# Kernel optimization log

Hardware: AMD Instinct MI355X
Metric: run time of the kernel (lower is better)

## Reference

```python
import jax, jax.numpy as jnp
import numpy as np

N = 20000   # nodes
E = 320000  # directed edges (before self-loops)
D = 64      # input_dim
H = 10      # GAT heads
HD = H * D  # 640
NEG_SLOPE = 0.2


def setup_inputs() -> dict:
    key = jax.random.key(0)
    ks = jax.random.split(key, 10)
    return {
        "x": jax.random.normal(ks[0], (N, D), jnp.float32),
        "W_gat": jax.random.normal(ks[1], (D, HD), jnp.float32) / np.sqrt(D).astype(np.float32),
        "att_src": jax.random.normal(ks[2], (H, D), jnp.float32) / np.sqrt(D).astype(np.float32),
        "att_dst": jax.random.normal(ks[3], (H, D), jnp.float32) / np.sqrt(D).astype(np.float32),
        "b_gat": jnp.zeros((HD,), jnp.float32),
        "W_gcn": jax.random.normal(ks[4], (HD, HD), jnp.float32) / np.sqrt(HD).astype(np.float32),
        "b_gcn": jnp.zeros((HD,), jnp.float32),
        "W1": jax.random.normal(ks[5], (2 * HD, 1500), jnp.float32) / np.sqrt(2 * HD).astype(np.float32),
        "b1": jnp.zeros((1500,), jnp.float32),
        "W2": jax.random.normal(ks[6], (1500, 10), jnp.float32) / np.sqrt(1500).astype(np.float32),
        "b2": jnp.zeros((10,), jnp.float32),
        "edge_index": jax.random.randint(ks[7], (2, E), 0, N, dtype=jnp.int64),
    }


def _forward(x, W_gat, att_src, att_dst, b_gat, W_gcn, b_gcn, W1, b1, W2, b2, edge_index):
    n = x.shape[0]
    # add self-loops (PyG default for both GATConv and GCNConv)
    loop = jnp.arange(n, dtype=edge_index.dtype)
    ei = jnp.concatenate([edge_index, jnp.stack([loop, loop])], axis=1)
    src, dst = ei[0], ei[1]

    # ---- GATConv(D -> D, heads=H, concat) ----
    xl = (x @ W_gat).reshape(n, H, D)                      # [N,H,D]
    a_src = jnp.einsum('nhd,hd->nh', xl, att_src)          # [N,H]
    a_dst = jnp.einsum('nhd,hd->nh', xl, att_dst)          # [N,H]
    alpha = jax.nn.leaky_relu(a_src[src] + a_dst[dst], NEG_SLOPE)  # [E',H]
    m = jax.ops.segment_max(alpha, dst, num_segments=n)    # segment softmax over incoming edges
    ex = jnp.exp(alpha - m[dst])
    den = jax.ops.segment_sum(ex, dst, num_segments=n)
    w = ex / (den[dst] + 1e-16)                            # [E',H]
    msg = xl[src] * w[:, :, None]                          # [E',H,D]
    x1 = jax.ops.segment_sum(msg, dst, num_segments=n).reshape(n, HD) + b_gat
    x1 = jax.nn.relu(x1)

    # ---- GCNConv(HD -> HD), symmetric norm with self-loops ----
    deg = jax.ops.segment_sum(jnp.ones(ei.shape[1], x.dtype), dst, num_segments=n)
    dinv = jnp.where(deg > 0, jax.lax.rsqrt(deg), 0.0)
    norm = dinv[src] * dinv[dst]                           # [E']
    xw = x1 @ W_gcn                                        # [N,HD]
    x2 = jax.ops.segment_sum(xw[src] * norm[:, None], dst, num_segments=n) + b_gcn
    x2 = jax.nn.relu(x2)

    # ---- global max/mean pool (batch=None -> single graph) + MLP head ----
    pooled = jnp.concatenate([x2.max(axis=0, keepdims=True),
                              x2.mean(axis=0, keepdims=True)], axis=1)  # [1, 2*HD]
    h = jax.nn.relu(pooled @ W1 + b1)
    # dropout is identity in eval mode
    return h @ W2 + b2                                     # [1, 10]


def reference(x, W_gat, att_src, att_dst, b_gat, W_gcn, b_gcn, W1, b1, W2, b2, edge_index):
    return _forward(x, W_gat, att_src, att_dst, b_gat, W_gcn, b_gcn, W1, b1, W2, b2, edge_index)
```

## Files before the change

kernel.cpp:

```cpp
#include <hip/hip_runtime.h>
#include <hip/hip_bf16.h>
#include <math.h>

#define NN 20000
#define DD 64
#define HH 10
#define HDIM 640
#define NEG 0.2f
#define H1 1500
#define ASTRIDE 12
#define BKK 128

typedef _Float16 half8 __attribute__((ext_vector_type(8)));
typedef _Float16 half4v __attribute__((ext_vector_type(4)));
typedef _Float16 half2v __attribute__((ext_vector_type(2)));
typedef float f32x4 __attribute__((ext_vector_type(4)));

__global__ __launch_bounds__(256) void k_cvtT(const float* __restrict__ W,
                                              _Float16* __restrict__ WT,
                                              int rows, int cols)
{
    __shared__ float t[32][33];
    const int bx = blockIdx.x, by = blockIdx.y;
    const int lx = threadIdx.x & 31, ly = threadIdx.x >> 5;
    #pragma unroll
    for (int i = ly; i < 32; i += 8)
        t[i][lx] = W[(size_t)(by * 32 + i) * cols + bx * 32 + lx];
    __syncthreads();
    #pragma unroll
    for (int j = ly; j < 32; j += 8)
        WT[(size_t)(bx * 32 + j) * rows + by * 32 + lx] = (_Float16)t[lx][j];
}

__global__ __launch_bounds__(256) void k_gemm1(
    const float* __restrict__ x, const _Float16* __restrict__ WgT,
    const float* __restrict__ att_s, const float* __restrict__ att_d,
    _Float16* __restrict__ xl, float* __restrict__ a_src, float* __restrict__ a_dst)
{
    __shared__ _Float16 As[128][72];
    __shared__ _Float16 Bs[64][72];
    const int tid = threadIdx.x;
    const int m0 = blockIdx.x * 128;
    const int h  = blockIdx.y;
    const int n0 = h * 64;

    {
        const int row = tid >> 1, ch = (tid & 1) * 32;
        const int gr = m0 + row;
        if (gr < NN) {
            const float* xp = &x[(size_t)gr * DD + ch];
            #pragma unroll
            for (int i = 0; i < 8; ++i) {
                const float4 v = *(const float4*)&xp[i * 4];
                half4v o = {(_Float16)v.x, (_Float16)v.y, (_Float16)v.z, (_Float16)v.w};
                *(half4v*)&As[row][ch + i * 4] = o;
            }
        } else {
            const half8 z = {0, 0, 0, 0, 0, 0, 0, 0};
            #pragma unroll
            for (int i = 0; i < 4; ++i) *(half8*)&As[row][ch + i * 8] = z;
        }
    }
    {
        const int row = tid >> 2, part = (tid & 3) * 16;
        const _Float16* wp = &WgT[(size_t)(n0 + row) * DD + part];
        *(half8*)&Bs[row][part]     = *(const half8*)&wp[0];
        *(half8*)&Bs[row][part + 8] = *(const half8*)&wp[8];
    }
    __syncthreads();

    const int lane = tid & 63, wave = tid >> 6;
    const int l15 = lane & 15, quad = lane >> 4;
    f32x4 acc[2][4];
    #pragma unroll
    for (int r = 0; r < 2; ++r)
        #pragma unroll
        for (int c = 0; c < 4; ++c) acc[r][c] = (f32x4){0.f, 0.f, 0.f, 0.f};

    #pragma unroll
    for (int ks = 0; ks < 2; ++ks) {
        const half8 a0 = *(const half8*)&As[wave * 32 + l15][ks * 32 + quad * 8];
        const half8 a1 = *(const half8*)&As[wave * 32 + 16 + l15][ks * 32 + quad * 8];
        #pragma unroll
        for (int c = 0; c < 4; ++c) {
            const half8 b = *(const half8*)&Bs[c * 16 + l15][ks * 32 + quad * 8];
            acc[0][c] = __builtin_amdgcn_mfma_f32_16x16x32_f16(a0, b, acc[0][c], 0, 0, 0);
            acc[1][c] = __builtin_amdgcn_mfma_f32_16x16x32_f16(a1, b, acc[1][c], 0, 0, 0);
        }
    }

    float asv[4], adv[4];
    #pragma unroll
    for (int c = 0; c < 4; ++c) {
        asv[c] = att_s[h * DD + c * 16 + l15];
        adv[c] = att_d[h * DD + c * 16 + l15];
    }
    #pragma unroll
    for (int r = 0; r < 2; ++r) {
        float ps[4] = {0.f, 0.f, 0.f, 0.f}, pd[4] = {0.f, 0.f, 0.f, 0.f};
        #pragma unroll
        for (int c = 0; c < 4; ++c)
            #pragma unroll
            for (int g = 0; g < 4; ++g) {
                ps[g] = fmaf(acc[r][c][g], asv[c], ps[g]);
                pd[g] = fmaf(acc[r][c][g], adv[c], pd[g]);
            }
        #pragma unroll
        for (int m = 1; m <= 8; m <<= 1)
            #pragma unroll
            for (int g = 0; g < 4; ++g) {
                ps[g] += __shfl_xor(ps[g], m);
                pd[g] += __shfl_xor(pd[g], m);
            }
        #pragma unroll
        for (int c = 0; c < 4; ++c)
            #pragma unroll
            for (int g = 0; g < 4; ++g) {
                const int row = m0 + wave * 32 + r * 16 + quad * 4 + g;
                if (row < NN)
                    xl[(size_t)row * HDIM + n0 + c * 16 + l15] = (_Float16)acc[r][c][g];
            }
        if (l15 == 0)
            #pragma unroll
            for (int g = 0; g < 4; ++g) {
                const int row = m0 + wave * 32 + r * 16 + quad * 4 + g;
                if (row < NN) {
                    a_src[(size_t)row * ASTRIDE + h] = ps[g];
                    a_dst[(size_t)row * ASTRIDE + h] = pd[g];
                }
            }
    }
}

__global__ void k_count(const int* __restrict__ ei, int E, int* __restrict__ cnt)
{
    const int e = blockIdx.x * blockDim.x + threadIdx.x;
    if (e >= E + NN) return;
    const int d = (e < E) ? ei[E + e] : (e - E);
    atomicAdd(&cnt[d], 1);
}

__global__ __launch_bounds__(1024) void k_scan(const int* __restrict__ cnt,
                                               int* __restrict__ rowptr,
                                               float* __restrict__ dinv)
{
    __shared__ int sh[1024];
    const int t = threadIdx.x;
    const int CH = 20;
    const int base = t * CH;
    int loc[CH];
    int s = 0;
    #pragma unroll
    for (int i = 0; i < CH; ++i) {
        const int idx = base + i;
        const int c = (idx < NN) ? cnt[idx] : 0;
        loc[i] = s; s += c;
    }
    sh[t] = s; __syncthreads();
    for (int off = 1; off < 1024; off <<= 1) {
        const int v = (t >= off) ? sh[t - off] : 0;
        __syncthreads();
        sh[t] += v;
        __syncthreads();
    }
    const int prev = (t == 0) ? 0 : sh[t - 1];
    #pragma unroll
    for (int i = 0; i < CH; ++i) {
        const int idx = base + i;
        if (idx < NN) {
            rowptr[idx] = prev + loc[i];
            dinv[idx]   = rsqrtf((float)cnt[idx]);
        }
    }
    if (t == 1023) rowptr[NN] = sh[1023];
}

__global__ void k_fill(const int* __restrict__ ei, int E,
                       const int* __restrict__ rowptr,
                       int* __restrict__ cursor, int* __restrict__ csr,
                       int* __restrict__ dstv,
                       const float* __restrict__ dinv, float* __restrict__ wn)
{
    const int e = blockIdx.x * blockDim.x + threadIdx.x;
    if (e >= E + NN) return;
    int s, d;
    if (e < E) { s = ei[e]; d = ei[E + e]; } else { s = d = e - E; }
    const int pos = atomicAdd(&cursor[d], 1);
    const int idx = rowptr[d] + pos;
    csr[idx]  = s;
    dstv[idx] = d;
    wn[idx]   = dinv[s] * dinv[d];
}

__global__ void k_stat(const int* __restrict__ csr, const int* __restrict__ dstv,
                       const float* __restrict__ aS, const float* __restrict__ aD,
                       float* __restrict__ wgat, int EP)
{
    const int j = blockIdx.x * blockDim.x + threadIdx.x;
    if (j >= EP) return;
    const int s = csr[j], d = dstv[j];
    const f32x4 s0 = *(const f32x4*)&aS[(size_t)s * ASTRIDE];
    const f32x4 s1 = *(const f32x4*)&aS[(size_t)s * ASTRIDE + 4];
    const float2 s2 = *(const float2*)&aS[(size_t)s * ASTRIDE + 8];
    const f32x4 d0 = *(const f32x4*)&aD[(size_t)d * ASTRIDE];
    const f32x4 d1 = *(const f32x4*)&aD[(size_t)d * ASTRIDE + 4];
    const float2 d2 = *(const float2*)&aD[(size_t)d * ASTRIDE + 8];
    const float av[10] = {s0.x + d0.x, s0.y + d0.y, s0.z + d0.z, s0.w + d0.w,
                          s1.x + d1.x, s1.y + d1.y, s1.z + d1.z, s1.w + d1.w,
                          s2.x + d2.x, s2.y + d2.y};
    float* wp = &wgat[(size_t)j * HH];
    #pragma unroll
    for (int h = 0; h < 10; ++h) {
        float a = av[h];
        a = (a >= 0.f) ? a : NEG * a;
        wp[h] = __expf(a);
    }
}

__global__ __launch_bounds__(256) void k_gat_gather(
    const int* __restrict__ rowptr, const int* __restrict__ csr,
    const float* __restrict__ wgat, const _Float16* __restrict__ xl,
    const float* __restrict__ b_gat, _Float16* __restrict__ x1)
{
    const int wave = threadIdx.x >> 6, lane = threadIdx.x & 63;
    const int n = blockIdx.x * 4 + wave;
    const int c0 = lane * 8;
    const int h0 = lane >> 3;
    const bool dual = (lane < 16);
    const int c1 = 512 + lane * 8;
    const int h1 = 8 + (lane >> 3);

    float acc0[8], acc1[8], ws0 = 0.f, ws1 = 0.f;
    #pragma unroll
    for (int i = 0; i < 8; ++i) { acc0[i] = 0.f; acc1[i] = 0.f; }

    const int j0 = rowptr[n], j1 = rowptr[n + 1];
    int j = j0;
    for (; j + 3 < j1; j += 4) {
        const int sA = csr[j], sB = csr[j + 1], sC = csr[j + 2], sD = csr[j + 3];
        const float wA0 = wgat[(size_t)(j + 0) * HH + h0];
        const float wB0 = wgat[(size_t)(j + 1) * HH + h0];
        const float wC0 = wgat[(size_t)(j + 2) * HH + h0];
        const float wD0 = wgat[(size_t)(j + 3) * HH + h0];
        ws0 += wA0 + wB0 + wC0 + wD0;
        const half8 vA0 = *(const half8*)&xl[(size_t)sA * HDIM + c0];
        const half8 vB0 = *(const half8*)&xl[(size_t)sB * HDIM + c0];
        const half8 vC0 = *(const half8*)&xl[(size_t)sC * HDIM + c0];
        const half8 vD0 = *(const half8*)&xl[(size_t)sD * HDIM + c0];
        #pragma unroll
        for (int i = 0; i < 8; ++i) {
            acc0[i] = fmaf(wA0, (float)vA0[i], acc0[i]);
            acc0[i] = fmaf(wB0, (float)vB0[i], acc0[i]);
            acc0[i] = fmaf(wC0, (float)vC0[i], acc0[i]);
            acc0[i] = fmaf(wD0, (float)vD0[i], acc0[i]);
        }
        if (dual) {
            const float wA1 = wgat[(size_t)(j + 0) * HH + h1];
            const float wB1 = wgat[(size_t)(j + 1) * HH + h1];
            const float wC1 = wgat[(size_t)(j + 2) * HH + h1];
            const float wD1 = wgat[(size_t)(j + 3) * HH + h1];
            ws1 += wA1 + wB1 + wC1 + wD1;
            const half8 vA1 = *(const half8*)&xl[(size_t)sA * HDIM + c1];
            const half8 vB1 = *(const half8*)&xl[(size_t)sB * HDIM + c1];
            const half8 vC1 = *(const half8*)&xl[(size_t)sC * HDIM + c1];
            const half8 vD1 = *(const half8*)&xl[(size_t)sD * HDIM + c1];
            #pragma unroll
            for (int i = 0; i < 8; ++i) {
                acc1[i] = fmaf(wA1, (float)vA1[i], acc1[i]);
                acc1[i] = fmaf(wB1, (float)vB1[i], acc1[i]);
                acc1[i] = fmaf(wC1, (float)vC1[i], acc1[i]);
                acc1[i] = fmaf(wD1, (float)vD1[i], acc1[i]);
            }
        }
    }
    for (; j < j1; ++j) {
        const int sA = csr[j];
        const float wA0 = wgat[(size_t)j * HH + h0];
        ws0 += wA0;
        const half8 vA0 = *(const half8*)&xl[(size_t)sA * HDIM + c0];
        #pragma unroll
        for (int i = 0; i < 8; ++i) acc0[i] = fmaf(wA0, (float)vA0[i], acc0[i]);
        if (dual) {
            const float wA1 = wgat[(size_t)j * HH + h1];
            ws1 += wA1;
            const half8 vA1 = *(const half8*)&xl[(size_t)sA * HDIM + c1];
            #pragma unroll
            for (int i = 0; i < 8; ++i) acc1[i] = fmaf(wA1, (float)vA1[i], acc1[i]);
        }
    }

    {
        const float rr = 1.f / (ws0 + 1e-16f);
        const float4 ba = *(const float4*)&b_gat[c0];
        const float4 bb = *(const float4*)&b_gat[c0 + 4];
        const float bv[8] = {ba.x, ba.y, ba.z, ba.w, bb.x, bb.y, bb.z, bb.w};
        half8 o;
        #pragma unroll
        for (int i = 0; i < 8; ++i) {
            const float v = fmaf(acc0[i], rr, bv[i]);
            o[i] = (_Float16)((v > 0.f) ? v : 0.f);
        }
        *(half8*)&x1[(size_t)n * HDIM + c0] = o;
    }
    if (dual) {
        const float rr = 1.f / (ws1 + 1e-16f);
        const float4 ba = *(const float4*)&b_gat[c1];
        const float4 bb = *(const float4*)&b_gat[c1 + 4];
        const float bv[8] = {ba.x, ba.y, ba.z, ba.w, bb.x, bb.y, bb.z, bb.w};
        half8 o;
        #pragma unroll
        for (int i = 0; i < 8; ++i) {
            const float v = fmaf(acc1[i], rr, bv[i]);
            o[i] = (_Float16)((v > 0.f) ? v : 0.f);
        }
        *(half8*)&x1[(size_t)n * HDIM + c1] = o;
    }
}

__global__ __launch_bounds__(256) void k_gemm2(const _Float16* __restrict__ X,
                                               const _Float16* __restrict__ Wbt,
                                               _Float16* __restrict__ Y)
{
    __shared__ _Float16 Bs[128 * BKK];
    const int tid = threadIdx.x;
    const int lane = tid & 63, wave = tid >> 6;
    const int l15 = lane & 15, quad = lane >> 4;
    const int m0 = blockIdx.x * 128 + wave * 32;
    const int n0 = blockIdx.y * 128;
    const int l7 = l15 & 7;

    f32x4 acc[2][8];
    #pragma unroll
    for (int r = 0; r < 2; ++r)
        #pragma unroll
        for (int c = 0; c < 8; ++c) acc[r][c] = (f32x4){0.f, 0.f, 0.f, 0.f};

    const int jrow = lane >> 4;
    const int jchunk = lane & 15;

    const _Float16* a0p = &X[(size_t)(m0 + l15) * HDIM + quad * 8];
    const _Float16* a1p = a0p + (size_t)16 * HDIM;

    for (int kb = 0; kb < HDIM; kb += BKK) {
        #pragma unroll
        for (int i = 0; i < 8; ++i) {
            const int r = (wave * 8 + i) * 4 + jrow;
            const int ck = jchunk ^ (r & 7);
            const _Float16* src = &Wbt[(size_t)(n0 + r) * HDIM + kb + ck * 8];
            __builtin_amdgcn_global_load_lds(
                (const __attribute__((address_space(1))) void*)src,
                (__attribute__((address_space(3))) void*)&Bs[(size_t)(wave * 8 + i) * 512],
                16, 0, 0);
        }
        half8 a0[4], a1[4];
        #pragma unroll
        for (int ks = 0; ks < 4; ++ks) {
            a0[ks] = *(const half8*)(a0p + kb + ks * 32);
            a1[ks] = *(const half8*)(a1p + kb + ks * 32);
        }
        __syncthreads();
        #pragma unroll
        for (int ks = 0; ks < 4; ++ks) {
            #pragma unroll
            for (int c = 0; c < 8; ++c) {
                const int br = c * 16 + l15;
                const int ck = (4 * ks + quad) ^ l7;
                const half8 b = *(const half8*)&Bs[(size_t)br * BKK + ck * 8];
                acc[0][c] = __builtin_amdgcn_mfma_f32_16x16x32_f16(a0[ks], b, acc[0][c], 0, 0, 0);
                acc[1][c] = __builtin_amdgcn_mfma_f32_16x16x32_f16(a1[ks], b, acc[1][c], 0, 0, 0);
            }
        }
        __syncthreads();
    }

    #pragma unroll
    for (int r = 0; r < 2; ++r) {
        #pragma unroll
        for (int c = 0; c < 8; ++c) {
            #pragma unroll
            for (int g = 0; g < 4; ++g) {
                const int row = m0 + r * 16 + quad * 4 + g;
                if (row < NN)
                    Y[(size_t)row * HDIM + n0 + c * 16 + l15] = (_Float16)acc[r][c][g];
            }
        }
    }
}

__global__ __launch_bounds__(256) void k_gcn_gather(
    const int* __restrict__ rowptr, const int* __restrict__ csr,
    const float* __restrict__ wn, const _Float16* __restrict__ xw,
    const float* __restrict__ b_gcn, _Float16* __restrict__ x2)
{
    const int wave = threadIdx.x >> 6, lane = threadIdx.x & 63;
    const int n = blockIdx.x * 4 + wave;
    const int c0 = lane * 8;
    const bool dual = (lane < 16);
    const int c1 = 512 + lane * 8;

    float acc0[8], acc1[8];
    #pragma unroll
    for (int i = 0; i < 8; ++i) { acc0[i] = 0.f; acc1[i] = 0.f; }

    const int j0 = rowptr[n], j1 = rowptr[n + 1];
    int j = j0;
    for (; j + 3 < j1; j += 4) {
        const int sA = csr[j], sB = csr[j + 1], sC = csr[j + 2], sD = csr[j + 3];
        const float wA = wn[j], wB = wn[j + 1], wC = wn[j + 2], wD = wn[j + 3];
        const half8 vA0 = *(const half8*)&xw[(size_t)sA * HDIM + c0];
        const half8 vB0 = *(const half8*)&xw[(size_t)sB * HDIM + c0];
        const half8 vC0 = *(const half8*)&xw[(size_t)sC * HDIM + c0];
        const half8 vD0 = *(const half8*)&xw[(size_t)sD * HDIM + c0];
        #pragma unroll
        for (int i = 0; i < 8; ++i) {
            acc0[i] = fmaf(wA, (float)vA0[i], acc0[i]);
            acc0[i] = fmaf(wB, (float)vB0[i], acc0[i]);
            acc0[i] = fmaf(wC, (float)vC0[i], acc0[i]);
            acc0[i] = fmaf(wD, (float)vD0[i], acc0[i]);
        }
        if (dual) {
            const half8 vA1 = *(const half8*)&xw[(size_t)sA * HDIM + c1];
            const half8 vB1 = *(const half8*)&xw[(size_t)sB * HDIM + c1];
            const half8 vC1 = *(const half8*)&xw[(size_t)sC * HDIM + c1];
            const half8 vD1 = *(const half8*)&xw[(size_t)sD * HDIM + c1];
            #pragma unroll
            for (int i = 0; i < 8; ++i) {
                acc1[i] = fmaf(wA, (float)vA1[i], acc1[i]);
                acc1[i] = fmaf(wB, (float)vB1[i], acc1[i]);
                acc1[i] = fmaf(wC, (float)vC1[i], acc1[i]);
                acc1[i] = fmaf(wD, (float)vD1[i], acc1[i]);
            }
        }
    }
    for (; j < j1; ++j) {
        const int sA = csr[j];
        const float wA = wn[j];
        const half8 vA0 = *(const half8*)&xw[(size_t)sA * HDIM + c0];
        #pragma unroll
        for (int i = 0; i < 8; ++i) acc0[i] = fmaf(wA, (float)vA0[i], acc0[i]);
        if (dual) {
            const half8 vA1 = *(const half8*)&xw[(size_t)sA * HDIM + c1];
            #pragma unroll
            for (int i = 0; i < 8; ++i) acc1[i] = fmaf(wA, (float)vA1[i], acc1[i]);
        }
    }

    {
        const float4 ba = *(const float4*)&b_gcn[c0];
        const float4 bb = *(const float4*)&b_gcn[c0 + 4];
        const float bv[8] = {ba.x, ba.y, ba.z, ba.w, bb.x, bb.y, bb.z, bb.w};
        half8 o;
        #pragma unroll
        for (int i = 0; i < 8; ++i) {
            const float v = acc0[i] + bv[i];
            o[i] = (_Float16)((v > 0.f) ? v : 0.f);
        }
        *(half8*)&x2[(size_t)n * HDIM + c0] = o;
    }
    if (dual) {
        const float4 ba = *(const float4*)&b_gcn[c1];
        const float4 bb = *(const float4*)&b_gcn[c1 + 4];
        const float bv[8] = {ba.x, ba.y, ba.z, ba.w, bb.x, bb.y, bb.z, bb.w};
        half8 o;
        #pragma unroll
        for (int i = 0; i < 8; ++i) {
            const float v = acc1[i] + bv[i];
            o[i] = (_Float16)((v > 0.f) ? v : 0.f);
        }
        *(half8*)&x2[(size_t)n * HDIM + c1] = o;
    }
}

__global__ __launch_bounds__(64) void k_pool(const _Float16* __restrict__ x2,
                                             float* __restrict__ pmax,
                                             float* __restrict__ psum)
{
    const int t = threadIdx.x;
    const int col = blockIdx.x * 128 + t * 2;
    const int nb = blockIdx.y;
    float mx0 = 0.f, mx1 = 0.f, s0 = 0.f, s1 = 0.f;
    const int nend = nb * 250 + 250;
    for (int n = nb * 250; n < nend; ++n) {
        const half2v v = *(const half2v*)&x2[(size_t)n * HDIM + col];
        const float v0 = (float)v.x, v1 = (float)v.y;
        mx0 = fmaxf(mx0, v0); mx1 = fmaxf(mx1, v1);
        s0 += v0; s1 += v1;
    }
    atomicMax((int*)&pmax[col],     __float_as_int(mx0));
    atomicMax((int*)&pmax[col + 1], __float_as_int(mx1));
    atomicAdd(&psum[col],     s0);
    atomicAdd(&psum[col + 1], s1);
}

__global__ __launch_bounds__(256) void k_mlp1(const float* __restrict__ pmax,
                                              const float* __restrict__ psum,
                                              const float* __restrict__ W1,
                                              float* __restrict__ hacc)
{
    __shared__ float pl[80];
    const int t = threadIdx.x;
    const int i0 = blockIdx.y * 80;
    if (t < 80) {
        const int i = i0 + t;
        pl[t] = (i < HDIM) ? pmax[i] : psum[i - HDIM] * (1.0f / NN);
    }
    __syncthreads();
    const int j = blockIdx.x * 256 + t;
    if (j >= H1) return;
    float acc = 0.f;
    #pragma unroll 8
    for (int i = 0; i < 80; ++i)
        acc = fmaf(pl[i], W1[(size_t)(i0 + i) * H1 + j], acc);
    atomicAdd(&hacc[j], acc);
}

__global__ __launch_bounds__(256) void k_mlp2(const float* __restrict__ hacc,
                                              const float* __restrict__ b1,
                                              const float* __restrict__ W2,
                                              const float* __restrict__ b2,
                                              float* __restrict__ out)
{
    __shared__ float hsh[H1];
    __shared__ float red[256];
    const int t = threadIdx.x;
    for (int i = t; i < H1; i += 256) {
        const float v = hacc[i] + b1[i];
        hsh[i] = (v > 0.f) ? v : 0.f;
    }
    __syncthreads();
    float acc[10];
    #pragma unroll
    for (int k = 0; k < 10; ++k) acc[k] = 0.f;
    for (int i = t; i < H1; i += 256) {
        const float h = hsh[i];
        #pragma unroll
        for (int k = 0; k < 10; ++k) acc[k] = fmaf(h, W2[i * 10 + k], acc[k]);
    }
    for (int k = 0; k < 10; ++k) {
        red[t] = acc[k]; __syncthreads();
        for (int s2 = 128; s2 > 0; s2 >>= 1) {
            if (t < s2) red[t] += red[t + s2];
            __syncthreads();
        }
        if (t == 0) out[k] = red[0] + b2[k];
        __syncthreads();
    }
}

extern "C" void kernel_launch(void* const* d_in, const int* in_sizes, int n_in,
                              void* d_out, int out_size, void* d_ws, size_t ws_size,
                              hipStream_t stream)
{
    const float* x     = (const float*)d_in[0];
    const float* Wg    = (const float*)d_in[1];
    const float* att_s = (const float*)d_in[2];
    const float* att_d = (const float*)d_in[3];
    const float* b_gat = (const float*)d_in[4];
    const float* Wgcn  = (const float*)d_in[5];
    const float* b_gcn = (const float*)d_in[6];
    const float* W1    = (const float*)d_in[7];
    const float* b1    = (const float*)d_in[8];
    const float* W2    = (const float*)d_in[9];
    const float* b2    = (const float*)d_in[10];
    const int*   ei    = (const int*)d_in[11];
    const int E = in_sizes[11] / 2;
    const int EP = E + NN;
    float* out = (float*)d_out;

    char* wsp = (char*)d_ws;
    size_t off = 0;
    auto alc = [&](size_t b) { void* p = wsp + off; off += (b + 255) & ~(size_t)255; return p; };
    _Float16* bufA = (_Float16*)alc((size_t)NN * HDIM * 2);
    _Float16* bufB = (_Float16*)alc((size_t)NN * HDIM * 2);
    float* aS     = (float*)alc((size_t)NN * ASTRIDE * 4);
    float* aD     = (float*)alc((size_t)NN * ASTRIDE * 4);
    int*   rowptr = (int*)alc((size_t)(NN + 1) * 4);
    int*   csr    = (int*)alc((size_t)EP * 4);
    int*   dstv   = (int*)alc((size_t)EP * 4);
    float* dinv   = (float*)alc((size_t)NN * 4);
    float* wn     = (float*)alc((size_t)EP * 4);
    float* wgat   = (float*)alc((size_t)EP * HH * 4);
    _Float16* Wbt = (_Float16*)alc((size_t)HDIM * HDIM * 2);
    _Float16* WgT = (_Float16*)alc((size_t)HDIM * DD * 2);
    const size_t zoff = off;
    int*   cnt    = (int*)alc((size_t)NN * 4);
    int*   cursor = (int*)alc((size_t)NN * 4);
    float* pmax   = (float*)alc((size_t)HDIM * 4);
    float* psum   = (float*)alc((size_t)HDIM * 4);
    float* hacc   = (float*)alc((size_t)H1 * 4);
    const size_t zsize = off - zoff;

    hipMemsetAsync(cnt, 0, zsize, stream);

    k_count<<<(EP + 255) / 256, 256, 0, stream>>>(ei, E, cnt);
    k_scan<<<1, 1024, 0, stream>>>(cnt, rowptr, dinv);
    k_fill<<<(EP + 255) / 256, 256, 0, stream>>>(ei, E, rowptr, cursor, csr, dstv, dinv, wn);
    dim3 gw1(HDIM / 32, HDIM / 32);
    k_cvtT<<<gw1, 256, 0, stream>>>(Wgcn, Wbt, HDIM, HDIM);
    dim3 gw2(HDIM / 32, DD / 32);
    k_cvtT<<<gw2, 256, 0, stream>>>(Wg, WgT, DD, HDIM);
    dim3 g1((NN + 127) / 128, HH);
    k_gemm1<<<g1, 256, 0, stream>>>(x, WgT, att_s, att_d, bufA, aS, aD);
    k_stat<<<(EP + 255) / 256, 256, 0, stream>>>(csr, dstv, aS, aD, wgat, EP);
    k_gat_gather<<<NN / 4, 256, 0, stream>>>(rowptr, csr, wgat, bufA, b_gat, bufB);
    dim3 g2((NN + 127) / 128, HDIM / 128);
    k_gemm2<<<g2, 256, 0, stream>>>(bufB, Wbt, bufA);
    k_gcn_gather<<<NN / 4, 256, 0, stream>>>(rowptr, csr, wn, bufA, b_gcn, bufB);
    dim3 gp(HDIM / 128, 80);
    k_pool<<<gp, 64, 0, stream>>>(bufB, pmax, psum);
    dim3 gm1(6, 16);
    k_mlp1<<<gm1, 256, 0, stream>>>(pmax, psum, W1, hacc);
    k_mlp2<<<1, 256, 0, stream>>>(hacc, b1, W2, b2, out);
}
```

Baseline: 388.1 us.

## Fuse edge-score computation into CSR fill, merge weight converts, unroll gathers by 8

```diff
diff --git a/kernel.cpp b/kernel.cpp
--- a/kernel.cpp
+++ b/kernel.cpp
@@ -16,12 +16,17 @@
 typedef _Float16 half2v __attribute__((ext_vector_type(2)));
 typedef float f32x4 __attribute__((ext_vector_type(4)));
 
-__global__ __launch_bounds__(256) void k_cvtT(const float* __restrict__ W,
-                                              _Float16* __restrict__ WT,
-                                              int rows, int cols)
+__global__ __launch_bounds__(256) void k_cvtB(const float* __restrict__ Wgcn,
+                                              const float* __restrict__ Wg,
+                                              _Float16* __restrict__ Wbt,
+                                              _Float16* __restrict__ WgT)
 {
     __shared__ float t[32][33];
-    const int bx = blockIdx.x, by = blockIdx.y;
+    const int bx = blockIdx.x;
+    int by = blockIdx.y;
+    const float* W; _Float16* WT; int rows, cols;
+    if (by < 20) { W = Wgcn; WT = Wbt; rows = HDIM; cols = HDIM; }
+    else         { W = Wg;   WT = WgT; rows = DD;   cols = HDIM; by -= 20; }
     const int lx = threadIdx.x & 31, ly = threadIdx.x >> 5;
     #pragma unroll
     for (int i = ly; i < 32; i += 8)
@@ -178,8 +183,9 @@
 __global__ void k_fill(const int* __restrict__ ei, int E,
                        const int* __restrict__ rowptr,
                        int* __restrict__ cursor, int* __restrict__ csr,
-                       int* __restrict__ dstv,
-                       const float* __restrict__ dinv, float* __restrict__ wn)
+                       const float* __restrict__ dinv, float* __restrict__ wn,
+                       const float* __restrict__ aS, const float* __restrict__ aD,
+                       float* __restrict__ wgat)
 {
     const int e = blockIdx.x * blockDim.x + threadIdx.x;
     if (e >= E + NN) return;
@@ -187,18 +193,9 @@
     if (e < E) { s = ei[e]; d = ei[E + e]; } else { s = d = e - E; }
     const int pos = atomicAdd(&cursor[d], 1);
     const int idx = rowptr[d] + pos;
-    csr[idx]  = s;
-    dstv[idx] = d;
-    wn[idx]   = dinv[s] * dinv[d];
-}
-
-__global__ void k_stat(const int* __restrict__ csr, const int* __restrict__ dstv,
-                       const float* __restrict__ aS, const float* __restrict__ aD,
-                       float* __restrict__ wgat, int EP)
-{
-    const int j = blockIdx.x * blockDim.x + threadIdx.x;
-    if (j >= EP) return;
-    const int s = csr[j], d = dstv[j];
+    csr[idx] = s;
+    wn[idx]  = dinv[s] * dinv[d];
+
     const f32x4 s0 = *(const f32x4*)&aS[(size_t)s * ASTRIDE];
     const f32x4 s1 = *(const f32x4*)&aS[(size_t)s * ASTRIDE + 4];
     const float2 s2 = *(const float2*)&aS[(size_t)s * ASTRIDE + 8];
@@ -208,7 +205,7 @@
     const float av[10] = {s0.x + d0.x, s0.y + d0.y, s0.z + d0.z, s0.w + d0.w,
                           s1.x + d1.x, s1.y + d1.y, s1.z + d1.z, s1.w + d1.w,
                           s2.x + d2.x, s2.y + d2.y};
-    float* wp = &wgat[(size_t)j * HH];
+    float* wp = &wgat[(size_t)idx * HH];
     #pragma unroll
     for (int h = 0; h < 10; ++h) {
         float a = av[h];
@@ -236,41 +233,34 @@
 
     const int j0 = rowptr[n], j1 = rowptr[n + 1];
     int j = j0;
-    for (; j + 3 < j1; j += 4) {
-        const int sA = csr[j], sB = csr[j + 1], sC = csr[j + 2], sD = csr[j + 3];
-        const float wA0 = wgat[(size_t)(j + 0) * HH + h0];
-        const float wB0 = wgat[(size_t)(j + 1) * HH + h0];
-        const float wC0 = wgat[(size_t)(j + 2) * HH + h0];
-        const float wD0 = wgat[(size_t)(j + 3) * HH + h0];
-        ws0 += wA0 + wB0 + wC0 + wD0;
-        const half8 vA0 = *(const half8*)&xl[(size_t)sA * HDIM + c0];
-        const half8 vB0 = *(const half8*)&xl[(size_t)sB * HDIM + c0];
-        const half8 vC0 = *(const half8*)&xl[(size_t)sC * HDIM + c0];
-        const half8 vD0 = *(const half8*)&xl[(size_t)sD * HDIM + c0];
-        #pragma unroll
-        for (int i = 0; i < 8; ++i) {
-            acc0[i] = fmaf(wA0, (float)vA0[i], acc0[i]);
-            acc0[i] = fmaf(wB0, (float)vB0[i], acc0[i]);
-            acc0[i] = fmaf(wC0, (float)vC0[i], acc0[i]);
-            acc0[i] = fmaf(wD0, (float)vD0[i], acc0[i]);
-        }
+    for (; j + 7 < j1; j += 8) {
+        int s[8]; float w0[8];
+        #pragma unroll
+        for (int u = 0; u < 8; ++u) {
+            s[u]  = csr[j + u];
+            w0[u] = wgat[(size_t)(j + u) * HH + h0];
+            ws0  += w0[u];
+        }
+        half8 v0[8];
+        #pragma unroll
+        for (int u = 0; u < 8; ++u) v0[u] = *(const half8*)&xl[(size_t)s[u] * HDIM + c0];
+        #pragma unroll
+        for (int u = 0; u < 8; ++u)
+            #pragma unroll
+            for (int i = 0; i < 8; ++i) acc0[i] = fmaf(w0[u], (float)v0[u][i], acc0[i]);
         if (dual) {
-            const float wA1 = wgat[(size_t)(j + 0) * HH + h1];
-            const float wB1 = wgat[(size_t)(j + 1) * HH + h1];
-            const float wC1 = wgat[(size_t)(j + 2) * HH + h1];
-            const float wD1 = wgat[(size_t)(j + 3) * HH + h1];
-            ws1 += wA1 + wB1 + wC1 + wD1;
-            const half8 vA1 = *(const half8*)&xl[(size_t)sA * HDIM + c1];
-            const half8 vB1 = *(const half8*)&xl[(size_t)sB * HDIM + c1];
-            const half8 vC1 = *(const half8*)&xl[(size_t)sC * HDIM + c1];
-            const half8 vD1 = *(const half8*)&xl[(size_t)sD * HDIM + c1];
-            #pragma unroll
-            for (int i = 0; i < 8; ++i) {
-                acc1[i] = fmaf(wA1, (float)vA1[i], acc1[i]);
-                acc1[i] = fmaf(wB1, (float)vB1[i], acc1[i]);
-                acc1[i] = fmaf(wC1, (float)vC1[i], acc1[i]);
-                acc1[i] = fmaf(wD1, (float)vD1[i], acc1[i]);
-            }
+            float w1[8];
+            half8 v1[8];
+            #pragma unroll
+            for (int u = 0; u < 8; ++u) {
+                w1[u] = wgat[(size_t)(j + u) * HH + h1];
+                ws1  += w1[u];
+                v1[u] = *(const half8*)&xl[(size_t)s[u] * HDIM + c1];
+            }
+            #pragma unroll
+            for (int u = 0; u < 8; ++u)
+                #pragma unroll
+                for (int i = 0; i < 8; ++i) acc1[i] = fmaf(w1[u], (float)v1[u][i], acc1[i]);
         }
     }
     for (; j < j1; ++j) {
@@ -404,32 +394,25 @@
 
     const int j0 = rowptr[n], j1 = rowptr[n + 1];
     int j = j0;
-    for (; j + 3 < j1; j += 4) {
-        const int sA = csr[j], sB = csr[j + 1], sC = csr[j + 2], sD = csr[j + 3];
-        const float wA = wn[j], wB = wn[j + 1], wC = wn[j + 2], wD = wn[j + 3];
-        const half8 vA0 = *(const half8*)&xw[(size_t)sA * HDIM + c0];
-        const half8 vB0 = *(const half8*)&xw[(size_t)sB * HDIM + c0];
-        const half8 vC0 = *(const half8*)&xw[(size_t)sC * HDIM + c0];
-        const half8 vD0 = *(const half8*)&xw[(size_t)sD * HDIM + c0];
-        #pragma unroll
-        for (int i = 0; i < 8; ++i) {
-            acc0[i] = fmaf(wA, (float)vA0[i], acc0[i]);
-            acc0[i] = fmaf(wB, (float)vB0[i], acc0[i]);
-            acc0[i] = fmaf(wC, (float)vC0[i], acc0[i]);
-            acc0[i] = fmaf(wD, (float)vD0[i], acc0[i]);
-        }
+    for (; j + 7 < j1; j += 8) {
+        int s[8]; float w[8];
+        #pragma unroll
+        for (int u = 0; u < 8; ++u) { s[u] = csr[j + u]; w[u] = wn[j + u]; }
+        half8 v0[8];
+        #pragma unroll
+        for (int u = 0; u < 8; ++u) v0[u] = *(const half8*)&xw[(size_t)s[u] * HDIM + c0];
+        #pragma unroll
+        for (int u = 0; u < 8; ++u)
+            #pragma unroll
+            for (int i = 0; i < 8; ++i) acc0[i] = fmaf(w[u], (float)v0[u][i], acc0[i]);
         if (dual) {
-            const half8 vA1 = *(const half8*)&xw[(size_t)sA * HDIM + c1];
-            const half8 vB1 = *(const half8*)&xw[(size_t)sB * HDIM + c1];
-            const half8 vC1 = *(const half8*)&xw[(size_t)sC * HDIM + c1];
-            const half8 vD1 = *(const half8*)&xw[(size_t)sD * HDIM + c1];
-            #pragma unroll
-            for (int i = 0; i < 8; ++i) {
-                acc1[i] = fmaf(wA, (float)vA1[i], acc1[i]);
-                acc1[i] = fmaf(wB, (float)vB1[i], acc1[i]);
-                acc1[i] = fmaf(wC, (float)vC1[i], acc1[i]);
-                acc1[i] = fmaf(wD, (float)vD1[i], acc1[i]);
-            }
+            half8 v1[8];
+            #pragma unroll
+            for (int u = 0; u < 8; ++u) v1[u] = *(const half8*)&xw[(size_t)s[u] * HDIM + c1];
+            #pragma unroll
+            for (int u = 0; u < 8; ++u)
+                #pragma unroll
+                for (int i = 0; i < 8; ++i) acc1[i] = fmaf(w[u], (float)v1[u][i], acc1[i]);
         }
     }
     for (; j < j1; ++j) {
@@ -576,7 +559,6 @@
     float* aD     = (float*)alc((size_t)NN * ASTRIDE * 4);
     int*   rowptr = (int*)alc((size_t)(NN + 1) * 4);
     int*   csr    = (int*)alc((size_t)EP * 4);
-    int*   dstv   = (int*)alc((size_t)EP * 4);
     float* dinv   = (float*)alc((size_t)NN * 4);
     float* wn     = (float*)alc((size_t)EP * 4);
     float* wgat   = (float*)alc((size_t)EP * HH * 4);
@@ -592,16 +574,14 @@
 
     hipMemsetAsync(cnt, 0, zsize, stream);
 
+    dim3 gw(HDIM / 32, HDIM / 32 + DD / 32);
+    k_cvtB<<<gw, 256, 0, stream>>>(Wgcn, Wg, Wbt, WgT);
+    dim3 g1((NN + 127) / 128, HH);
+    k_gemm1<<<g1, 256, 0, stream>>>(x, WgT, att_s, att_d, bufA, aS, aD);
     k_count<<<(EP + 255) / 256, 256, 0, stream>>>(ei, E, cnt);
     k_scan<<<1, 1024, 0, stream>>>(cnt, rowptr, dinv);
-    k_fill<<<(EP + 255) / 256, 256, 0, stream>>>(ei, E, rowptr, cursor, csr, dstv, dinv, wn);
-    dim3 gw1(HDIM / 32, HDIM / 32);
-    k_cvtT<<<gw1, 256, 0, stream>>>(Wgcn, Wbt, HDIM, HDIM);
-    dim3 gw2(HDIM / 32, DD / 32);
-    k_cvtT<<<gw2, 256, 0, stream>>>(Wg, WgT, DD, HDIM);
-    dim3 g1((NN + 127) / 128, HH);
-    k_gemm1<<<g1, 256, 0, stream>>>(x, WgT, att_s, att_d, bufA, aS, aD);
-    k_stat<<<(EP + 255) / 256, 256, 0, stream>>>(csr, dstv, aS, aD, wgat, EP);
+    k_fill<<<(EP + 255) / 256, 256, 0, stream>>>(ei, E, rowptr, cursor, csr,
+                                                 dinv, wn, aS, aD, wgat);
     k_gat_gather<<<NN / 4, 256, 0, stream>>>(rowptr, csr, wgat, bufA, b_gat, bufB);
     dim3 g2((NN + 127) / 128, HDIM / 128);
     k_gemm2<<<g2, 256, 0, stream>>>(bufB, Wbt, bufA);
```

Result: no change. 392.9 us (+1.2%).
